# Performance work log

Measured on AMD Instinct MI355X. Metric: run time of the kernel, lower is better.

Reference implementation:

```python
import jax, jax.numpy as jnp
import numpy as np

N_NODES = 100000
N_EDGES = 600000
DIMS = [128, 64, 32, 2]


def gcn_conv(x, edge_index, W, b, n_nodes):
    """PyG GCNConv (eval mode): symmetric-normalized aggregation with self-loops.
    out = D^{-1/2} (A + I) D^{-1/2} (x W) + b
    """
    h = x @ W  # [N, out] -- transform first (cheaper when out < in)
    src = jnp.concatenate([edge_index[0], jnp.arange(n_nodes)])  # add self-loops
    dst = jnp.concatenate([edge_index[1], jnp.arange(n_nodes)])
    deg = jax.ops.segment_sum(jnp.ones_like(dst, dtype=h.dtype), dst,
                              num_segments=n_nodes)  # in-degree incl. self-loop
    dinv = jax.lax.rsqrt(deg)
    norm = dinv[src] * dinv[dst]  # [E+N]
    msg = norm[:, None] * h[src]  # gather + scale
    out = jax.ops.segment_sum(msg, dst, num_segments=n_nodes)  # scatter-add
    return out + b


def setup_inputs() -> dict:
    key = jax.random.key(0)
    ks = jax.random.split(key, 8)
    x = jax.random.normal(ks[0], (N_NODES, DIMS[0]), dtype=jnp.float32)
    edge_index = jax.random.randint(ks[1], (2, N_EDGES), 0, N_NODES, dtype=jnp.int64)
    inp = {"x": x, "edge_index": edge_index}
    for i in range(3):
        fan_in, fan_out = DIMS[i], DIMS[i + 1]
        s = 1.0 / np.sqrt(fan_in)
        inp[f"W{i+1}"] = jax.random.uniform(ks[2 + 2 * i], (fan_in, fan_out),
                                            minval=-s, maxval=s, dtype=jnp.float32)
        inp[f"b{i+1}"] = jnp.zeros((fan_out,), dtype=jnp.float32)
    return inp


def reference(x, edge_index, W1, b1, W2, b2, W3, b3):
    # 3 stacked GCNConv layers with ReLU; dropout is identity in eval mode.
    n = x.shape[0]
    x = jax.nn.relu(gcn_conv(x, edge_index, W1, b1, n))
    x = jax.nn.relu(gcn_conv(x, edge_index, W2, b2, n))
    x = jax.nn.relu(gcn_conv(x, edge_index, W3, b3, n))
    return x
```

## Files before the change

### kernel.cpp

```cpp
#include <hip/hip_runtime.h>
#include <math.h>


#define FULL_GRID 2048
#define PARTS 8

typedef const __attribute__((address_space(1))) void* gas_ptr;
typedef __attribute__((address_space(3))) void* las_ptr;
typedef __attribute__((ext_vector_type(8))) short bf16x8;
typedef __attribute__((ext_vector_type(4))) float f32x4;

__device__ __forceinline__ void gld16(const void* g, void* l) {
  __builtin_amdgcn_global_load_lds((gas_ptr)g, (las_ptr)l, 16, 0, 0);
}

__device__ __forceinline__ unsigned short f2bf(float f) {
  unsigned int u = __float_as_uint(f);
  u += 0x7FFF + ((u >> 16) & 1);
  return (unsigned short)(u >> 16);
}
__device__ __forceinline__ float bf2f(unsigned short h) {
  return __uint_as_float(((unsigned int)h) << 16);
}

__global__ __launch_bounds__(256) void k_init(int* __restrict__ p, int n4,
                                              const unsigned int* __restrict__ words,
                                              int* __restrict__ flag) {
  if (blockIdx.x == gridDim.x - 1) {
    __shared__ int sm[256];
    int cnt = 0;
    #pragma unroll
    for (int j = 0; j < 8; ++j) {
      int idx = (threadIdx.x * 8 + j) * 2 + 1;
      cnt += (words[idx] == 0u) ? 1 : 0;
    }
    sm[threadIdx.x] = cnt;
    __syncthreads();
    for (int off = 128; off > 0; off >>= 1) {
      if (threadIdx.x < off) sm[threadIdx.x] += sm[threadIdx.x + off];
      __syncthreads();
    }
    if (threadIdx.x == 0) flag[0] = (sm[0] > 1024) ? 1 : 0;
    return;
  }
  int i = blockIdx.x * blockDim.x + threadIdx.x;
  const int stride = (gridDim.x - 1) * blockDim.x;
  int4* p4 = (int4*)p;
  for (; i < n4; i += stride) p4[i] = make_int4(0, 0, 0, 0);
}

__global__ __launch_bounds__(256) void k_prepw(const float* __restrict__ W1,
                                               const float* __restrict__ W2,
                                               short* __restrict__ Wh1,
                                               short* __restrict__ Wl1,
                                               short* __restrict__ Wh2,
                                               short* __restrict__ Wl2) {
  const int t = blockIdx.x * 256 + threadIdx.x;
  const int stride = gridDim.x * 256;
  for (int p = t; p < 4 * 4 * 64 * 8; p += stride) {
    const int e = p & 7, lane = (p >> 3) & 63, nt = (p >> 9) & 3, kt = p >> 11;
    const int k = kt * 32 + (lane >> 4) * 8 + e;
    const int nn = nt * 16 + (lane & 15);
    const float f = W1[k * 64 + nn];
    const unsigned short h = f2bf(f);
    Wh1[p] = (short)h;
    Wl1[p] = (short)f2bf(f - bf2f(h));
  }
  for (int p = t; p < 2 * 2 * 64 * 8; p += stride) {
    const int e = p & 7, lane = (p >> 3) & 63, nt = (p >> 9) & 1, kt = p >> 10;
    const int k = kt * 32 + (lane >> 4) * 8 + e;
    const int nn = nt * 16 + (lane & 15);
    const float f = W2[k * 32 + nn];
    const unsigned short h = f2bf(f);
    Wh2[p] = (short)h;
    Wl2[p] = (short)f2bf(f - bf2f(h));
  }
}

__global__ __launch_bounds__(256) void k_hist(const void* __restrict__ eraw, int E,
                                              int N, const int* __restrict__ flag,
                                              int* __restrict__ counts) {
  const int is64 = flag[0];
  const int part = blockIdx.x & (PARTS - 1);
  const int lo = (int)((long long)N * part / PARTS);
  const int hi = (int)((long long)N * (part + 1) / PARTS);
  int i = (blockIdx.x >> 3) * blockDim.x + threadIdx.x;
  const int stride = (gridDim.x >> 3) * blockDim.x;
  if (is64) {
    const long long* e = (const long long*)eraw;
    for (; i < E; i += stride) {
      const int d = (int)e[(long long)E + i];
      if (d >= lo && d < hi) atomicAdd(&counts[d], 1);
    }
  } else {
    const int* e = (const int*)eraw;
    for (; i < E; i += stride) {
      const int d = e[E + i];
      if (d >= lo && d < hi) atomicAdd(&counts[d], 1);
    }
  }
}

__global__ __launch_bounds__(1024) void k_scan1(const int* __restrict__ counts,
                                                int* __restrict__ scanned,
                                                int* __restrict__ partials, int n) {
  __shared__ int sm[1024];
  const int i = blockIdx.x * 1024 + threadIdx.x;
  const int v = (i < n) ? counts[i] : 0;
  sm[threadIdx.x] = v;
  __syncthreads();
  for (int off = 1; off < 1024; off <<= 1) {
    int t = sm[threadIdx.x];
    int u = (threadIdx.x >= off) ? sm[threadIdx.x - off] : 0;
    __syncthreads();
    sm[threadIdx.x] = t + u;
    __syncthreads();
  }
  const int inc = sm[threadIdx.x];
  if (i < n) scanned[i] = inc - v;
  if (threadIdx.x == 1023) partials[blockIdx.x] = inc;
}

__global__ __launch_bounds__(256) void k_scan3(const int* __restrict__ scanned,
                                               const int* __restrict__ partials,
                                               int nb,
                                               const int* __restrict__ counts,
                                               int* __restrict__ offsets,
                                               int* __restrict__ cursor,
                                               float* __restrict__ dinv, int n) {
  __shared__ int ps[1024];
  for (int t = threadIdx.x; t < nb; t += 256) ps[t] = partials[t];
  __syncthreads();
  if (threadIdx.x == 0) {
    int run = 0;
    for (int b = 0; b < nb; ++b) { const int v = ps[b]; ps[b] = run; run += v; }
  }
  __syncthreads();
  int i = blockIdx.x * blockDim.x + threadIdx.x;
  const int stride = gridDim.x * blockDim.x;
  for (; i < n; i += stride) {
    const int o = scanned[i] + ps[i >> 10];
    offsets[i] = o;
    cursor[i] = o;
    dinv[i] = rsqrtf((float)counts[i] + 1.0f);
  }
}

__global__ __launch_bounds__(256) void k_fill(const void* __restrict__ eraw, int E,
                                              int N, const int* __restrict__ flag,
                                              int* __restrict__ cursor,
                                              int* __restrict__ elist) {
  const int is64 = flag[0];
  const int part = blockIdx.x & (PARTS - 1);
  const int lo = (int)((long long)N * part / PARTS);
  const int hi = (int)((long long)N * (part + 1) / PARTS);
  int i = (blockIdx.x >> 3) * blockDim.x + threadIdx.x;
  const int stride = (gridDim.x >> 3) * blockDim.x;
  if (is64) {
    const long long* e = (const long long*)eraw;
    for (; i < E; i += stride) {
      const int d = (int)e[(long long)E + i];
      if (d >= lo && d < hi) {
        const int s = (int)e[i];
        elist[atomicAdd(&cursor[d], 1)] = s;
      }
    }
  } else {
    const int* e = (const int*)eraw;
    for (; i < E; i += stride) {
      const int d = e[E + i];
      if (d >= lo && d < hi) {
        const int s = e[i];
        elist[atomicAdd(&cursor[d], 1)] = s;
      }
    }
  }
}

template <int F_IN, int F_OUT>
__global__ __launch_bounds__(256) void k_transform_mfma(
    const float* __restrict__ X, const short* __restrict__ Wh,
    const short* __restrict__ Wl, const float* __restrict__ dinv,
    float* __restrict__ H, int n) {
  constexpr int KT = F_IN / 32;
  constexpr int NT = F_OUT / 16;
  constexpr int K4f = F_IN / 4;
  constexpr int SLOTS = F_IN / 8;
  constexpr int TILE_M = 64;
  constexpr int WFRAG = KT * NT * 64 * 8;
  static_assert((WFRAG * 2) % 1024 == 0, "W segs");

  __shared__ __align__(16) unsigned short Xh[TILE_M * F_IN];
  __shared__ __align__(16) unsigned short Xl[TILE_M * F_IN];
  __shared__ __align__(16) unsigned short Whs[WFRAG];
  __shared__ __align__(16) unsigned short Wls[WFRAG];

  const int tid = threadIdx.x;
  const int lane = tid & 63;
  const int wid = tid >> 6;
  const long long base = (long long)blockIdx.x * TILE_M;

  constexpr int WSEGS = WFRAG * 2 / 1024;
  for (int seg = wid; seg < WSEGS; seg += 4) {
    gld16((const char*)Wh + seg * 1024 + lane * 16, (char*)Whs + seg * 1024);
    gld16((const char*)Wl + seg * 1024 + lane * 16, (char*)Wls + seg * 1024);
  }

  const float4* __restrict__ X4 = (const float4*)X;
  for (int g = tid; g < TILE_M * K4f; g += 256) {
    const int row = g / K4f, c4 = g % K4f;
    float4 v = make_float4(0.f, 0.f, 0.f, 0.f);
    if (base + row < n) v = X4[(base + row) * K4f + c4];
    ushort4 hv, lv;
    hv.x = f2bf(v.x); lv.x = f2bf(v.x - bf2f(hv.x));
    hv.y = f2bf(v.y); lv.y = f2bf(v.y - bf2f(hv.y));
    hv.z = f2bf(v.z); lv.z = f2bf(v.z - bf2f(hv.z));
    hv.w = f2bf(v.w); lv.w = f2bf(v.w - bf2f(hv.w));
    const int slot = (c4 >> 1) ^ (row & (SLOTS - 1));
    const int boff = row * (F_IN * 2) + slot * 16 + (c4 & 1) * 8;
    *(ushort4*)((char*)Xh + boff) = hv;
    *(ushort4*)((char*)Xl + boff) = lv;
  }
  __syncthreads();

  const int arow = lane & 15;
  const int kg = lane >> 4;
  const int lrow = wid * 16 + arow;

  f32x4 acc[NT];
  #pragma unroll
  for (int t = 0; t < NT; ++t) {
    f32x4 z = {0.f, 0.f, 0.f, 0.f};
    acc[t] = z;
  }

  #pragma unroll
  for (int kt = 0; kt < KT; ++kt) {
    const int slot = (kt * 4 + kg) ^ (lrow & (SLOTS - 1));
    const int aoff = lrow * (F_IN * 2) + slot * 16;
    const bf16x8 ah = *(const bf16x8*)((const char*)Xh + aoff);
    const bf16x8 al = *(const bf16x8*)((const char*)Xl + aoff);
    #pragma unroll
    for (int nt = 0; nt < NT; ++nt) {
      const int woff = ((kt * NT + nt) * 64 + lane) * 8;
      const bf16x8 bh = *(const bf16x8*)&Whs[woff];
      const bf16x8 bl = *(const bf16x8*)&Wls[woff];
      acc[nt] = __builtin_amdgcn_mfma_f32_16x16x32_bf16(ah, bh, acc[nt], 0, 0, 0);
      acc[nt] = __builtin_amdgcn_mfma_f32_16x16x32_bf16(ah, bl, acc[nt], 0, 0, 0);
      acc[nt] = __builtin_amdgcn_mfma_f32_16x16x32_bf16(al, bh, acc[nt], 0, 0, 0);
    }
  }

  #pragma unroll
  for (int r = 0; r < 4; ++r) {
    const long long row = base + wid * 16 + kg * 4 + r;
    if (row < n) {
      const float di = dinv[row];
      #pragma unroll
      for (int nt = 0; nt < NT; ++nt)
        H[row * F_OUT + nt * 16 + arow] = di * acc[nt][r];
    }
  }
}

template <int F, bool RELU_OUT, bool FUSE_W3>
__global__ __launch_bounds__(256) void k_agg_vec(const float* __restrict__ HS,
                                                 const float* __restrict__ dinv,
                                                 const int* __restrict__ offsets,
                                                 const int* __restrict__ counts,
                                                 const int* __restrict__ elist,
                                                 const float* __restrict__ bias,
                                                 const float* __restrict__ W3,
                                                 float* __restrict__ out, int n) {
  constexpr int LPE = F / 4;
  constexpr int EPW = 64 / LPE;
  const int lane = threadIdx.x & 63;
  const int wv = (blockIdx.x * (blockDim.x >> 6)) + (threadIdx.x >> 6);
  const int nwaves = gridDim.x * (blockDim.x >> 6);
  const int g = lane / LPE;
  const int fl = lane % LPE;
  const float4 bf = *(const float4*)&bias[fl * 4];

  float w3a0 = 0.f, w3a1 = 0.f, w3a2 = 0.f, w3a3 = 0.f;
  float w3b0 = 0.f, w3b1 = 0.f, w3b2 = 0.f, w3b3 = 0.f;
  if (FUSE_W3) {
    w3a0 = W3[(fl * 4 + 0) * 2 + 0]; w3b0 = W3[(fl * 4 + 0) * 2 + 1];
    w3a1 = W3[(fl * 4 + 1) * 2 + 0]; w3b1 = W3[(fl * 4 + 1) * 2 + 1];
    w3a2 = W3[(fl * 4 + 2) * 2 + 0]; w3b2 = W3[(fl * 4 + 2) * 2 + 1];
    w3a3 = W3[(fl * 4 + 3) * 2 + 0]; w3b3 = W3[(fl * 4 + 3) * 2 + 1];
  }

  for (long long d = wv; d < n; d += nwaves) {
    const float di = dinv[d];
    const int start = offsets[d];
    const int cnt = counts[d];
    float4 acc = make_float4(0.f, 0.f, 0.f, 0.f);
    if (g == 0) acc = *(const float4*)&HS[d * F + fl * 4];

    for (int j = 0; j < cnt; j += 2 * EPW) {
      const int e0 = j + g;
      const int e1 = j + EPW + g;
      const int i0 = elist[start + (e0 < cnt ? e0 : cnt - 1)];
      const int i1 = elist[start + (e1 < cnt ? e1 : cnt - 1)];
      const float4 v0 = *(const float4*)&HS[(long long)i0 * F + fl * 4];
      const float4 v1 = *(const float4*)&HS[(long long)i1 * F + fl * 4];
      if (e0 < cnt) {
        acc.x += v0.x; acc.y += v0.y; acc.z += v0.z; acc.w += v0.w;
      }
      if (e1 < cnt) {
        acc.x += v1.x; acc.y += v1.y; acc.z += v1.z; acc.w += v1.w;
      }
    }
    #pragma unroll
    for (int m = LPE; m < 64; m <<= 1) {
      acc.x += __shfl_xor(acc.x, m, 64);
      acc.y += __shfl_xor(acc.y, m, 64);
      acc.z += __shfl_xor(acc.z, m, 64);
      acc.w += __shfl_xor(acc.w, m, 64);
    }
    float4 r;
    r.x = fmaf(di, acc.x, bf.x);
    r.y = fmaf(di, acc.y, bf.y);
    r.z = fmaf(di, acc.z, bf.z);
    r.w = fmaf(di, acc.w, bf.w);
    if (RELU_OUT) {
      r.x = fmaxf(r.x, 0.f); r.y = fmaxf(r.y, 0.f);
      r.z = fmaxf(r.z, 0.f); r.w = fmaxf(r.w, 0.f);
    }
    if (!FUSE_W3) {
      if (g == 0) *(float4*)&out[d * F + fl * 4] = r;
    } else {
      float t0 = r.x * w3a0 + r.y * w3a1 + r.z * w3a2 + r.w * w3a3;
      float t1 = r.x * w3b0 + r.y * w3b1 + r.z * w3b2 + r.w * w3b3;
      #pragma unroll
      for (int m = 1; m < LPE; m <<= 1) {
        t0 += __shfl_xor(t0, m, 64);
        t1 += __shfl_xor(t1, m, 64);
      }
      if (lane == 0) {
        out[d * 2 + 0] = di * t0;
        out[d * 2 + 1] = di * t1;
      }
    }
  }
}

template <int F, bool RELU_OUT>
__global__ __launch_bounds__(256) void k_aggregate(const float* __restrict__ HS,
                                                   const float* __restrict__ dinv,
                                                   const int* __restrict__ offsets,
                                                   const int* __restrict__ counts,
                                                   const int* __restrict__ elist,
                                                   const float* __restrict__ bias,
                                                   float* __restrict__ out, int n) {
  const int f = threadIdx.x % F;
  const int grp = threadIdx.x / F;
  constexpr int GRPS = 256 / F;
  const float bf = bias[f];

  for (long long d = (long long)blockIdx.x * GRPS + grp; d < n;
       d += (long long)gridDim.x * GRPS) {
    const float di = dinv[d];
    float acc = HS[d * F + f];
    const int start = offsets[d];
    const int cnt = counts[d];
    for (int j = 0; j < cnt; j += 8) {
      int idx[8];
      float v[8];
      #pragma unroll
      for (int t = 0; t < 8; ++t) {
        const int jj = (j + t < cnt) ? (j + t) : j;
        idx[t] = elist[start + jj];
      }
      #pragma unroll
      for (int t = 0; t < 8; ++t) v[t] = HS[(long long)idx[t] * F + f];
      #pragma unroll
      for (int t = 0; t < 8; ++t) acc += (j + t < cnt) ? v[t] : 0.f;
    }
    float r = fmaf(di, acc, bf);
    if (RELU_OUT) r = fmaxf(r, 0.f);
    out[d * F + f] = r;
  }
}

extern "C" void kernel_launch(void* const* d_in, const int* in_sizes, int n_in,
                              void* d_out, int out_size, void* d_ws, size_t ws_size,
                              hipStream_t stream) {
  const float* x = (const float*)d_in[0];
  const void* eraw = d_in[1];
  const float* W1 = (const float*)d_in[2];
  const float* b1 = (const float*)d_in[3];
  const float* W2 = (const float*)d_in[4];
  const float* b2 = (const float*)d_in[5];
  const float* W3 = (const float*)d_in[6];
  const float* b3 = (const float*)d_in[7];
  float* out = (float*)d_out;

  const int N = in_sizes[0] / 128;
  const int E = in_sizes[1] / 2;

  char* ws = (char*)d_ws;
  size_t off = 0;
  auto alloc = [&](size_t bytes) -> char* {
    char* p = ws + off;
    off = (off + bytes + 255) & ~(size_t)255;
    return p;
  };
  int*   flag     = (int*)alloc(256);
  int*   counts   = (int*)alloc((size_t)N * 4 + 16);
  int*   scanned  = (int*)alloc((size_t)N * 4);
  int*   partials = (int*)alloc(1024 * 4);
  int*   offsets  = (int*)alloc((size_t)N * 4);
  int*   cursor   = (int*)alloc((size_t)N * 4);
  int*   elist    = (int*)alloc((size_t)E * 4);
  float* dinv     = (float*)alloc((size_t)N * 4);
  short* Wh1      = (short*)alloc(4 * 4 * 64 * 8 * 2);
  short* Wl1      = (short*)alloc(4 * 4 * 64 * 8 * 2);
  short* Wh2      = (short*)alloc(2 * 2 * 64 * 8 * 2);
  short* Wl2      = (short*)alloc(2 * 2 * 64 * 8 * 2);
  float* hbuf     = (float*)alloc((size_t)N * 64 * 4);
  float* obuf     = (float*)alloc((size_t)N * 64 * 4);
  float* h2buf    = (float*)alloc((size_t)N * 32 * 4);
  (void)ws_size; (void)n_in; (void)out_size;

  k_init<<<129, 256, 0, stream>>>(counts, (N + 3) / 4, (const unsigned int*)eraw,
                                  flag);
  k_prepw<<<32, 256, 0, stream>>>(W1, W2, Wh1, Wl1, Wh2, Wl2);
  k_hist<<<FULL_GRID, 256, 0, stream>>>(eraw, E, N, flag, counts);
  const int NB = (N + 1023) >> 10;
  k_scan1<<<NB, 1024, 0, stream>>>(counts, scanned, partials, N);
  k_scan3<<<(N + 255) / 256, 256, 0, stream>>>(scanned, partials, NB, counts,
                                               offsets, cursor, dinv, N);
  k_fill<<<FULL_GRID, 256, 0, stream>>>(eraw, E, N, flag, cursor, elist);

  k_transform_mfma<128, 64><<<(N + 63) / 64, 256, 0, stream>>>(
      x, Wh1, Wl1, dinv, hbuf, N);
  k_agg_vec<64, true, false><<<FULL_GRID, 256, 0, stream>>>(
      hbuf, dinv, offsets, counts, elist, b1, nullptr, obuf, N);

  k_transform_mfma<64, 32><<<(N + 63) / 64, 256, 0, stream>>>(
      obuf, Wh2, Wl2, dinv, h2buf, N);
  k_agg_vec<32, true, true><<<FULL_GRID, 256, 0, stream>>>(
      h2buf, dinv, offsets, counts, elist, b2, W3, hbuf, N);

  k_aggregate<2, true><<<(N + 127) / 128, 256, 0, stream>>>(
      hbuf, dinv, offsets, counts, elist, b3, out, N);
}
```

Baseline: 172.3 us.

## Merge weight prep into init, pre-narrow edge indices, process two nodes per wave in aggregation

Folds the weight bf16 split kernel into the init kernel to drop one launch. Adds a kernel that converts int64 edge indices to int32 src/dst arrays once, so the histogram and fill passes read half the bytes. The vector aggregation now handles two destination nodes per wavefront per iteration, doubling the gathers in flight to hide latency. In exchange it adds an extra pass and buffer over the edges, raises register pressure, and wastes lanes when the two nodes' degrees differ.

```diff
diff --git a/kernel.cpp b/kernel.cpp
--- a/kernel.cpp
+++ b/kernel.cpp
@@ -25,8 +25,14 @@
 
 __global__ __launch_bounds__(256) void k_init(int* __restrict__ p, int n4,
                                               const unsigned int* __restrict__ words,
-                                              int* __restrict__ flag) {
-  if (blockIdx.x == gridDim.x - 1) {
+                                              int* __restrict__ flag,
+                                              const float* __restrict__ W1,
+                                              const float* __restrict__ W2,
+                                              short* __restrict__ Wh1,
+                                              short* __restrict__ Wl1,
+                                              short* __restrict__ Wh2,
+                                              short* __restrict__ Wl2) {
+  if (blockIdx.x == 128) {
     __shared__ int sm[256];
     int cnt = 0;
     #pragma unroll
@@ -43,61 +49,68 @@
     if (threadIdx.x == 0) flag[0] = (sm[0] > 1024) ? 1 : 0;
     return;
   }
+  if (blockIdx.x > 128) {
+    const int t = (blockIdx.x - 129) * 256 + threadIdx.x;
+    const int stride = 32 * 256;
+    for (int q = t; q < 4 * 4 * 64 * 8; q += stride) {
+      const int e = q & 7, lane = (q >> 3) & 63, nt = (q >> 9) & 3, kt = q >> 11;
+      const int k = kt * 32 + (lane >> 4) * 8 + e;
+      const int nn = nt * 16 + (lane & 15);
+      const float f = W1[k * 64 + nn];
+      const unsigned short h = f2bf(f);
+      Wh1[q] = (short)h;
+      Wl1[q] = (short)f2bf(f - bf2f(h));
+    }
+    for (int q = t; q < 2 * 2 * 64 * 8; q += stride) {
+      const int e = q & 7, lane = (q >> 3) & 63, nt = (q >> 9) & 1, kt = q >> 10;
+      const int k = kt * 32 + (lane >> 4) * 8 + e;
+      const int nn = nt * 16 + (lane & 15);
+      const float f = W2[k * 32 + nn];
+      const unsigned short h = f2bf(f);
+      Wh2[q] = (short)h;
+      Wl2[q] = (short)f2bf(f - bf2f(h));
+    }
+    return;
+  }
   int i = blockIdx.x * blockDim.x + threadIdx.x;
-  const int stride = (gridDim.x - 1) * blockDim.x;
+  const int stride = 128 * blockDim.x;
   int4* p4 = (int4*)p;
   for (; i < n4; i += stride) p4[i] = make_int4(0, 0, 0, 0);
 }
 
-__global__ __launch_bounds__(256) void k_prepw(const float* __restrict__ W1,
-                                               const float* __restrict__ W2,
-                                               short* __restrict__ Wh1,
-                                               short* __restrict__ Wl1,
-                                               short* __restrict__ Wh2,
-                                               short* __restrict__ Wl2) {
-  const int t = blockIdx.x * 256 + threadIdx.x;
-  const int stride = gridDim.x * 256;
-  for (int p = t; p < 4 * 4 * 64 * 8; p += stride) {
-    const int e = p & 7, lane = (p >> 3) & 63, nt = (p >> 9) & 3, kt = p >> 11;
-    const int k = kt * 32 + (lane >> 4) * 8 + e;
-    const int nn = nt * 16 + (lane & 15);
-    const float f = W1[k * 64 + nn];
-    const unsigned short h = f2bf(f);
-    Wh1[p] = (short)h;
-    Wl1[p] = (short)f2bf(f - bf2f(h));
-  }
-  for (int p = t; p < 2 * 2 * 64 * 8; p += stride) {
-    const int e = p & 7, lane = (p >> 3) & 63, nt = (p >> 9) & 1, kt = p >> 10;
-    const int k = kt * 32 + (lane >> 4) * 8 + e;
-    const int nn = nt * 16 + (lane & 15);
-    const float f = W2[k * 32 + nn];
-    const unsigned short h = f2bf(f);
-    Wh2[p] = (short)h;
-    Wl2[p] = (short)f2bf(f - bf2f(h));
-  }
-}
-
-__global__ __launch_bounds__(256) void k_hist(const void* __restrict__ eraw, int E,
-                                              int N, const int* __restrict__ flag,
-                                              int* __restrict__ counts) {
+__global__ __launch_bounds__(256) void k_normalize(const void* __restrict__ eraw,
+                                                   int E,
+                                                   const int* __restrict__ flag,
+                                                   int* __restrict__ srcn,
+                                                   int* __restrict__ dstn) {
   const int is64 = flag[0];
+  int i = blockIdx.x * blockDim.x + threadIdx.x;
+  const int stride = gridDim.x * blockDim.x;
+  if (is64) {
+    const long long* e = (const long long*)eraw;
+    for (; i < E; i += stride) {
+      srcn[i] = (int)e[i];
+      dstn[i] = (int)e[(long long)E + i];
+    }
+  } else {
+    const int* e = (const int*)eraw;
+    for (; i < E; i += stride) {
+      srcn[i] = e[i];
+      dstn[i] = e[E + i];
+    }
+  }
+}
+
+__global__ __launch_bounds__(256) void k_hist(const int* __restrict__ dstn, int E,
+                                              int N, int* __restrict__ counts) {
   const int part = blockIdx.x & (PARTS - 1);
   const int lo = (int)((long long)N * part / PARTS);
   const int hi = (int)((long long)N * (part + 1) / PARTS);
   int i = (blockIdx.x >> 3) * blockDim.x + threadIdx.x;
   const int stride = (gridDim.x >> 3) * blockDim.x;
-  if (is64) {
-    const long long* e = (const long long*)eraw;
-    for (; i < E; i += stride) {
-      const int d = (int)e[(long long)E + i];
-      if (d >= lo && d < hi) atomicAdd(&counts[d], 1);
-    }
-  } else {
-    const int* e = (const int*)eraw;
-    for (; i < E; i += stride) {
-      const int d = e[E + i];
-      if (d >= lo && d < hi) atomicAdd(&counts[d], 1);
-    }
+  for (; i < E; i += stride) {
+    const int d = dstn[i];
+    if (d >= lo && d < hi) atomicAdd(&counts[d], 1);
   }
 }
 
@@ -146,34 +159,18 @@
   }
 }
 
-__global__ __launch_bounds__(256) void k_fill(const void* __restrict__ eraw, int E,
-                                              int N, const int* __restrict__ flag,
-                                              int* __restrict__ cursor,
+__global__ __launch_bounds__(256) void k_fill(const int* __restrict__ srcn,
+                                              const int* __restrict__ dstn, int E,
+                                              int N, int* __restrict__ cursor,
                                               int* __restrict__ elist) {
-  const int is64 = flag[0];
   const int part = blockIdx.x & (PARTS - 1);
   const int lo = (int)((long long)N * part / PARTS);
   const int hi = (int)((long long)N * (part + 1) / PARTS);
   int i = (blockIdx.x >> 3) * blockDim.x + threadIdx.x;
   const int stride = (gridDim.x >> 3) * blockDim.x;
-  if (is64) {
-    const long long* e = (const long long*)eraw;
-    for (; i < E; i += stride) {
-      const int d = (int)e[(long long)E + i];
-      if (d >= lo && d < hi) {
-        const int s = (int)e[i];
-        elist[atomicAdd(&cursor[d], 1)] = s;
-      }
-    }
-  } else {
-    const int* e = (const int*)eraw;
-    for (; i < E; i += stride) {
-      const int d = e[E + i];
-      if (d >= lo && d < hi) {
-        const int s = e[i];
-        elist[atomicAdd(&cursor[d], 1)] = s;
-      }
-    }
+  for (; i < E; i += stride) {
+    const int d = dstn[i];
+    if (d >= lo && d < hi) elist[atomicAdd(&cursor[d], 1)] = srcn[i];
   }
 }
 
@@ -264,14 +261,14 @@
 }
 
 template <int F, bool RELU_OUT, bool FUSE_W3>
-__global__ __launch_bounds__(256) void k_agg_vec(const float* __restrict__ HS,
-                                                 const float* __restrict__ dinv,
-                                                 const int* __restrict__ offsets,
-                                                 const int* __restrict__ counts,
-                                                 const int* __restrict__ elist,
-                                                 const float* __restrict__ bias,
-                                                 const float* __restrict__ W3,
-                                                 float* __restrict__ out, int n) {
+__global__ __launch_bounds__(256) void k_agg_vec2(const float* __restrict__ HS,
+                                                  const float* __restrict__ dinv,
+                                                  const int* __restrict__ offsets,
+                                                  const int* __restrict__ counts,
+                                                  const int* __restrict__ elist,
+                                                  const float* __restrict__ bias,
+                                                  const float* __restrict__ W3,
+                                                  float* __restrict__ out, int n) {
   constexpr int LPE = F / 4;
   constexpr int EPW = 64 / LPE;
   const int lane = threadIdx.x & 63;
@@ -290,56 +287,91 @@
     w3a3 = W3[(fl * 4 + 3) * 2 + 0]; w3b3 = W3[(fl * 4 + 3) * 2 + 1];
   }
 
-  for (long long d = wv; d < n; d += nwaves) {
-    const float di = dinv[d];
-    const int start = offsets[d];
-    const int cnt = counts[d];
-    float4 acc = make_float4(0.f, 0.f, 0.f, 0.f);
-    if (g == 0) acc = *(const float4*)&HS[d * F + fl * 4];
-
-    for (int j = 0; j < cnt; j += 2 * EPW) {
+  for (long long dA = wv; dA < n; dA += 2ll * nwaves) {
+    const long long dB = dA + nwaves;
+    const bool hasB = dB < n;
+    const float diA = dinv[dA];
+    const float diB = hasB ? dinv[dB] : 0.f;
+    const int stA = offsets[dA];
+    const int cntA = counts[dA];
+    const int stB = hasB ? offsets[dB] : 0;
+    const int cntB = hasB ? counts[dB] : 0;
+    float4 accA = make_float4(0.f, 0.f, 0.f, 0.f);
+    float4 accB = make_float4(0.f, 0.f, 0.f, 0.f);
+    if (g == 0) accA = *(const float4*)&HS[dA * F + fl * 4];
+    if (g == 1 && hasB) accB = *(const float4*)&HS[dB * F + fl * 4];
+
+    const int jmax = cntA > cntB ? cntA : cntB;
+    const int cA = cntA > 0 ? cntA - 1 : 0;
+    const int cB = cntB > 0 ? cntB - 1 : 0;
+    for (int j = 0; j < jmax; j += 2 * EPW) {
       const int e0 = j + g;
       const int e1 = j + EPW + g;
-      const int i0 = elist[start + (e0 < cnt ? e0 : cnt - 1)];
-      const int i1 = elist[start + (e1 < cnt ? e1 : cnt - 1)];
-      const float4 v0 = *(const float4*)&HS[(long long)i0 * F + fl * 4];
-      const float4 v1 = *(const float4*)&HS[(long long)i1 * F + fl * 4];
-      if (e0 < cnt) {
-        acc.x += v0.x; acc.y += v0.y; acc.z += v0.z; acc.w += v0.w;
-      }
-      if (e1 < cnt) {
-        acc.x += v1.x; acc.y += v1.y; acc.z += v1.z; acc.w += v1.w;
+      const int iA0 = elist[stA + (e0 < cntA ? e0 : cA)];
+      const int iA1 = elist[stA + (e1 < cntA ? e1 : cA)];
+      const int iB0 = elist[stB + (e0 < cntB ? e0 : cB)];
+      const int iB1 = elist[stB + (e1 < cntB ? e1 : cB)];
+      const float4 vA0 = *(const float4*)&HS[(long long)iA0 * F + fl * 4];
+      const float4 vA1 = *(const float4*)&HS[(long long)iA1 * F + fl * 4];
+      const float4 vB0 = *(const float4*)&HS[(long long)iB0 * F + fl * 4];
+      const float4 vB1 = *(const float4*)&HS[(long long)iB1 * F + fl * 4];
+      if (e0 < cntA) {
+        accA.x += vA0.x; accA.y += vA0.y; accA.z += vA0.z; accA.w += vA0.w;
+      }
+      if (e1 < cntA) {
+        accA.x += vA1.x; accA.y += vA1.y; accA.z += vA1.z; accA.w += vA1.w;
+      }
+      if (e0 < cntB) {
+        accB.x += vB0.x; accB.y += vB0.y; accB.z += vB0.z; accB.w += vB0.w;
+      }
+      if (e1 < cntB) {
+        accB.x += vB1.x; accB.y += vB1.y; accB.z += vB1.z; accB.w += vB1.w;
       }
     }
     #pragma unroll
     for (int m = LPE; m < 64; m <<= 1) {
-      acc.x += __shfl_xor(acc.x, m, 64);
-      acc.y += __shfl_xor(acc.y, m, 64);
-      acc.z += __shfl_xor(acc.z, m, 64);
-      acc.w += __shfl_xor(acc.w, m, 64);
-    }
-    float4 r;
-    r.x = fmaf(di, acc.x, bf.x);
-    r.y = fmaf(di, acc.y, bf.y);
-    r.z = fmaf(di, acc.z, bf.z);
-    r.w = fmaf(di, acc.w, bf.w);
+      accA.x += __shfl_xor(accA.x, m, 64);
+      accA.y += __shfl_xor(accA.y, m, 64);
+      accA.z += __shfl_xor(accA.z, m, 64);
+      accA.w += __shfl_xor(accA.w, m, 64);
+      accB.x += __shfl_xor(accB.x, m, 64);
+      accB.y += __shfl_xor(accB.y, m, 64);
+      accB.z += __shfl_xor(accB.z, m, 64);
+      accB.w += __shfl_xor(accB.w, m, 64);
+    }
+    float4 rA, rB;
+    rA.x = fmaf(diA, accA.x, bf.x); rA.y = fmaf(diA, accA.y, bf.y);
+    rA.z = fmaf(diA, accA.z, bf.z); rA.w = fmaf(diA, accA.w, bf.w);
+    rB.x = fmaf(diB, accB.x, bf.x); rB.y = fmaf(diB, accB.y, bf.y);
+    rB.z = fmaf(diB, accB.z, bf.z); rB.w = fmaf(diB, accB.w, bf.w);
     if (RELU_OUT) {
-      r.x = fmaxf(r.x, 0.f); r.y = fmaxf(r.y, 0.f);
-      r.z = fmaxf(r.z, 0.f); r.w = fmaxf(r.w, 0.f);
+      rA.x = fmaxf(rA.x, 0.f); rA.y = fmaxf(rA.y, 0.f);
+      rA.z = fmaxf(rA.z, 0.f); rA.w = fmaxf(rA.w, 0.f);
+      rB.x = fmaxf(rB.x, 0.f); rB.y = fmaxf(rB.y, 0.f);
+      rB.z = fmaxf(rB.z, 0.f); rB.w = fmaxf(rB.w, 0.f);
     }
     if (!FUSE_W3) {
-      if (g == 0) *(float4*)&out[d * F + fl * 4] = r;
+      if (g == 0) *(float4*)&out[dA * F + fl * 4] = rA;
+      if (g == 1 && hasB) *(float4*)&out[dB * F + fl * 4] = rB;
     } else {
-      float t0 = r.x * w3a0 + r.y * w3a1 + r.z * w3a2 + r.w * w3a3;
-      float t1 = r.x * w3b0 + r.y * w3b1 + r.z * w3b2 + r.w * w3b3;
+      float tA0 = rA.x * w3a0 + rA.y * w3a1 + rA.z * w3a2 + rA.w * w3a3;
+      float tA1 = rA.x * w3b0 + rA.y * w3b1 + rA.z * w3b2 + rA.w * w3b3;
+      float tB0 = rB.x * w3a0 + rB.y * w3a1 + rB.z * w3a2 + rB.w * w3a3;
+      float tB1 = rB.x * w3b0 + rB.y * w3b1 + rB.z * w3b2 + rB.w * w3b3;
       #pragma unroll
       for (int m = 1; m < LPE; m <<= 1) {
-        t0 += __shfl_xor(t0, m, 64);
-        t1 += __shfl_xor(t1, m, 64);
+        tA0 += __shfl_xor(tA0, m, 64);
+        tA1 += __shfl_xor(tA1, m, 64);
+        tB0 += __shfl_xor(tB0, m, 64);
+        tB1 += __shfl_xor(tB1, m, 64);
       }
       if (lane == 0) {
-        out[d * 2 + 0] = di * t0;
-        out[d * 2 + 1] = di * t1;
+        out[dA * 2 + 0] = diA * tA0;
+        out[dA * 2 + 1] = diA * tA1;
+      }
+      if (lane == LPE && hasB) {
+        out[dB * 2 + 0] = diB * tB0;
+        out[dB * 2 + 1] = diB * tB1;
       }
     }
   }
@@ -412,6 +444,8 @@
   int*   partials = (int*)alloc(1024 * 4);
   int*   offsets  = (int*)alloc((size_t)N * 4);
   int*   cursor   = (int*)alloc((size_t)N * 4);
+  int*   srcn     = (int*)alloc((size_t)E * 4);
+  int*   dstn     = (int*)alloc((size_t)E * 4);
   int*   elist    = (int*)alloc((size_t)E * 4);
   float* dinv     = (float*)alloc((size_t)N * 4);
   short* Wh1      = (short*)alloc(4 * 4 * 64 * 8 * 2);
@@ -423,24 +457,24 @@
   float* h2buf    = (float*)alloc((size_t)N * 32 * 4);
   (void)ws_size; (void)n_in; (void)out_size;
 
-  k_init<<<129, 256, 0, stream>>>(counts, (N + 3) / 4, (const unsigned int*)eraw,
-                                  flag);
-  k_prepw<<<32, 256, 0, stream>>>(W1, W2, Wh1, Wl1, Wh2, Wl2);
-  k_hist<<<FULL_GRID, 256, 0, stream>>>(eraw, E, N, flag, counts);
+  k_init<<<161, 256, 0, stream>>>(counts, (N + 3) / 4, (const unsigned int*)eraw,
+                                  flag, W1, W2, Wh1, Wl1, Wh2, Wl2);
+  k_normalize<<<1024, 256, 0, stream>>>(eraw, E, flag, srcn, dstn);
+  k_hist<<<FULL_GRID, 256, 0, stream>>>(dstn, E, N, counts);
   const int NB = (N + 1023) >> 10;
   k_scan1<<<NB, 1024, 0, stream>>>(counts, scanned, partials, N);
   k_scan3<<<(N + 255) / 256, 256, 0, stream>>>(scanned, partials, NB, counts,
                                                offsets, cursor, dinv, N);
-  k_fill<<<FULL_GRID, 256, 0, stream>>>(eraw, E, N, flag, cursor, elist);
+  k_fill<<<FULL_GRID, 256, 0, stream>>>(srcn, dstn, E, N, cursor, elist);
 
   k_transform_mfma<128, 64><<<(N + 63) / 64, 256, 0, stream>>>(
       x, Wh1, Wl1, dinv, hbuf, N);
-  k_agg_vec<64, true, false><<<FULL_GRID, 256, 0, stream>>>(
+  k_agg_vec2<64, true, false><<<FULL_GRID, 256, 0, stream>>>(
       hbuf, dinv, offsets, counts, elist, b1, nullptr, obuf, N);
 
   k_transform_mfma<64, 32><<<(N + 63) / 64, 256, 0, stream>>>(
       obuf, Wh2, Wl2, dinv, h2buf, N);
-  k_agg_vec<32, true, true><<<FULL_GRID, 256, 0, stream>>>(
+  k_agg_vec2<32, true, true><<<FULL_GRID, 256, 0, stream>>>(
       h2buf, dinv, offsets, counts, elist, b2, W3, hbuf, N);
 
   k_aggregate<2, true><<<(N + 127) / 128, 256, 0, stream>>>(
```

After: 171.1 us. About the same (-0.7%).
